# Optimization experiments

Hardware: AMD Instinct MI355X
Metric: run time of the kernel (lower is better)

## Reference

```python
import jax, jax.numpy as jnp
import numpy as np

DISTANCE_SCALE = 25.0
VIEW_PE = 6
STEP = 0.02  # nominal ray-march step size used to scale dists


def positional_encoding(positions, freqs):
    # matches torch: (positions[..., None] * 2**k).reshape(..., freqs*C) -> [sin, cos]
    freq_bands = 2.0 ** jnp.arange(freqs, dtype=positions.dtype)
    pts = (positions[..., None] * freq_bands).reshape(positions.shape[:-1] + (freqs * positions.shape[-1],))
    return jnp.concatenate([jnp.sin(pts), jnp.cos(pts)], axis=-1)


def setup_inputs() -> dict:
    key = jax.random.key(0)
    ks = jax.random.split(key, 10)
    n_rays, n_samples, C, featureC = 4096, 256, 27, 128
    in_mlpC = 3 + 2 * VIEW_PE * 3 + C  # 66
    density_features = jax.random.normal(ks[0], (n_rays, n_samples), jnp.float32)
    app_features = jax.random.normal(ks[1], (n_rays, n_samples, C), jnp.float32)
    viewdirs = jax.random.normal(ks[2], (n_rays, 3), jnp.float32)
    viewdirs = viewdirs / jnp.linalg.norm(viewdirs, axis=-1, keepdims=True)
    dists = jax.random.uniform(ks[3], (n_rays, n_samples), jnp.float32) * STEP
    s1 = 1.0 / np.sqrt(in_mlpC)
    s2 = 1.0 / np.sqrt(featureC)
    W1 = jax.random.uniform(ks[4], (in_mlpC, featureC), jnp.float32, -s1, s1)
    b1 = jax.random.uniform(ks[5], (featureC,), jnp.float32, -s1, s1)
    W2 = jax.random.uniform(ks[6], (featureC, featureC), jnp.float32, -s2, s2)
    b2 = jax.random.uniform(ks[7], (featureC,), jnp.float32, -s2, s2)
    W3 = jax.random.uniform(ks[8], (featureC, 3), jnp.float32, -s2, s2)
    b3 = jnp.zeros((3,), jnp.float32)  # torch init: constant_(bias, 0)
    return {"density_features": density_features, "app_features": app_features,
            "viewdirs": viewdirs, "dists": dists,
            "W1": W1, "b1": b1, "W2": W2, "b2": b2, "W3": W3, "b3": b3}


def reference(density_features, app_features, viewdirs, dists, W1, b1, W2, b2, W3, b3):
    # feature2density (relu activation)
    sigma = jax.nn.relu(density_features)  # [R, S]
    # raw2alpha
    alpha = 1.0 - jnp.exp(-sigma * dists * DISTANCE_SCALE)  # [R, S]
    T = jnp.cumprod(jnp.concatenate([jnp.ones((alpha.shape[0], 1), alpha.dtype),
                                     1.0 - alpha + 1e-10], axis=-1), axis=-1)
    weights = alpha * T[:, :-1]  # [R, S]
    # radiance MLP over all sample points
    R, S, C = app_features.shape
    vd = jnp.broadcast_to(viewdirs[:, None, :], (R, S, 3))
    mlp_in = jnp.concatenate([app_features, vd, positional_encoding(vd, VIEW_PE)], axis=-1)  # [R,S,66]
    h = jax.nn.relu(mlp_in @ W1 + b1)
    h = jax.nn.relu(h @ W2 + b2)
    rgb = jax.nn.sigmoid(h @ W3 + b3)  # [R, S, 3]
    # composite (white background)
    acc_map = jnp.sum(weights, axis=-1)  # [R]
    rgb_map = jnp.einsum('rs,rsc->rc', weights, rgb)  # [R, 3]
    rgb_map = jnp.clip(rgb_map + (1.0 - acc_map[:, None]), 0.0, 1.0)
    return rgb_map
```

## Files before the change

### kernel.cpp

```cpp
#include <hip/hip_runtime.h>
#include <hip/hip_bf16.h>

typedef float f32x4 __attribute__((ext_vector_type(4)));
typedef short s16x8 __attribute__((ext_vector_type(8)));
typedef unsigned int u32;
typedef u32 u32x2 __attribute__((ext_vector_type(2)));

#define DIST_SCALE 25.0f

__device__ __forceinline__ unsigned short f2b(float f) {
  union { float f; unsigned u; } v; v.f = f;
  unsigned r = v.u + 0x7fffu + ((v.u >> 16) & 1u);
  return (unsigned short)(r >> 16);
}

__device__ __forceinline__ u32 cvtpk(float lo, float hi) {
  u32 r;
  asm("v_cvt_pk_bf16_f32 %0, %1, %2" : "=v"(r) : "v"(lo), "v"(hi));
  return r;
}

__device__ __forceinline__ int swzH(int s, int chbyte) {
  return (s * 256 + chbyte) ^ ((s & 7) << 4);
}

__global__ void prep_weights(const float* __restrict__ W1, const float* __restrict__ W2,
                             const float* __restrict__ W3, unsigned short* __restrict__ ws) {
  int t = blockIdx.x * 256 + threadIdx.x;
  int stride = gridDim.x * 256;
  for (int i = t; i < 128 * 32; i += stride) {
    int n = i >> 5, k = i & 31;
    ws[i] = (k < 27) ? f2b(W1[k * 128 + n]) : (unsigned short)0;
  }
  unsigned short* w2t = ws + 4096;
  for (int i = t; i < 128 * 128; i += stride) {
    int n = i >> 7, k = i & 127;
    w2t[i] = f2b(W2[k * 128 + n]);
  }
  unsigned short* w3p = ws + 4096 + 16384;
  for (int i = t; i < 4 * 16 * 32; i += stride) {
    int wv = i >> 9, rem = i & 511, n = rem >> 5, ks = rem & 31;
    int kg = ks >> 3, j = ks & 7;
    int ch = wv * 32 + ((j >> 2) << 4) + kg * 4 + (j & 3);
    w3p[i] = (n < 3) ? f2b(W3[ch * 3 + n]) : (unsigned short)0;
  }
}

__global__ void __attribute__((amdgpu_waves_per_eu(4, 4))) __launch_bounds__(256) nerf_main(
    const float* __restrict__ dens, const float* __restrict__ app,
    const float* __restrict__ vdirs, const float* __restrict__ dists,
    const float* __restrict__ W1, const float* __restrict__ b1,
    const float* __restrict__ b2v, const float* __restrict__ b3v,
    const unsigned short* __restrict__ wsb, float* __restrict__ out) {
  __shared__ unsigned short Xs[64 * 40];
  __shared__ unsigned short HA[64 * 128];
  __shared__ float part[4 * 4 * 16 * 4];
  __shared__ float wbuf[256];
  __shared__ float hcbuf[128];
  __shared__ float featbuf[40];
  __shared__ float red[4][4];

  const int t = threadIdx.x;
  const int lane = t & 63;
  const int wv = t >> 6;
  const int r = blockIdx.x;

  const unsigned short* W1aT = wsb;
  const unsigned short* W2T = wsb + 4096;
  const unsigned short* W3P = wsb + 4096 + 16384;
  char* HAb = (char*)HA;

  const int cl = lane & 15;
  const int kg = lane >> 4;
  const int chBase = wv * 32;

  for (int i = t; i < 1280; i += 256) ((u32*)Xs)[i] = 0u;
  if (t < 39) {
    float val;
    if (t < 3) val = vdirs[r * 3 + t];
    else {
      int jj = t - 3;
      int trig = jj / 18;
      int rem = jj % 18;
      int c = rem / 6, k = rem % 6;
      float v = vdirs[r * 3 + c] * (float)(1 << k);
      val = trig ? cosf(v) : sinf(v);
    }
    featbuf[t] = val;
  }
  if (wv == 0) {
    const float4 dv = *(const float4*)(dens + (size_t)r * 256 + lane * 4);
    const float4 tv = *(const float4*)(dists + (size_t)r * 256 + lane * 4);
    float f[4], al[4];
    float dl[4] = {dv.x, dv.y, dv.z, dv.w};
    float tl[4] = {tv.x, tv.y, tv.z, tv.w};
    float p = 1.0f;
#pragma unroll
    for (int q = 0; q < 4; ++q) {
      float sg = fmaxf(dl[q], 0.0f);
      float e = __expf(-sg * tl[q] * DIST_SCALE);
      al[q] = 1.0f - e;
      f[q] = e + 1e-10f;
      p *= f[q];
    }
    float P = p;
#pragma unroll
    for (int dlt = 1; dlt < 64; dlt <<= 1) {
      float v = __shfl_up(P, dlt, 64);
      if (lane >= dlt) P *= v;
    }
    float E = __shfl_up(P, 1, 64);
    if (lane == 0) E = 1.0f;
    float tr = E;
#pragma unroll
    for (int q = 0; q < 4; ++q) { wbuf[lane * 4 + q] = al[q] * tr; tr *= f[q]; }
  }
  __syncthreads();
  if (t < 128) {
    float s = b1[t];
    for (int j = 0; j < 39; ++j) s += featbuf[j] * W1[(27 + j) * 128 + t];
    hcbuf[t] = s;
  }

  s16x8 w1f[2], w2f[2][4], w3s;
#pragma unroll
  for (int nt = 0; nt < 2; ++nt)
    w1f[nt] = *(const s16x8*)(W1aT + (chBase + nt * 16 + cl) * 32 + kg * 8);
#pragma unroll
  for (int nt = 0; nt < 2; ++nt)
#pragma unroll
    for (int kk = 0; kk < 4; ++kk)
      w2f[nt][kk] = *(const s16x8*)(W2T + (chBase + nt * 16 + cl) * 128 + kk * 32 + kg * 8);
  w3s = *(const s16x8*)(W3P + wv * 512 + cl * 32 + kg * 8);

  __syncthreads();

  float pr = 0.0f, pg = 0.0f, pb = 0.0f, pw = 0.0f;
  const float b30 = b3v[0], b31 = b3v[1], b32 = b3v[2];
  const f32x4 hc0 = *(const f32x4*)(hcbuf + chBase + kg * 4);
  const f32x4 hc1 = *(const f32x4*)(hcbuf + chBase + 16 + kg * 4);
  const f32x4 bb0 = *(const f32x4*)(b2v + chBase + kg * 4);
  const f32x4 bb1 = *(const f32x4*)(b2v + chBase + 16 + kg * 4);

  const float* rayBase = app + (size_t)r * 256 * 27;
  f32x4 L0 = *(const f32x4*)(rayBase + 4 * t);
  f32x4 L1 = {};
  if (t < 176) L1 = *(const f32x4*)(rayBase + 4 * (t + 256));

  for (int chunk = 0; chunk < 4; ++chunk) {
    const int sBase = chunk * 64;
    {
      int e0 = 4 * t;
#pragma unroll
      for (int u = 0; u < 4; ++u) {
        unsigned e = e0 + u;
        unsigned s = e / 27u, c = e - s * 27u;
        *(unsigned short*)((char*)Xs + s * 80 + 2 * c) = f2b(L0[u]);
      }
      if (t < 176) {
        int e1 = 4 * (t + 256);
#pragma unroll
        for (int u = 0; u < 4; ++u) {
          unsigned e = e1 + u;
          unsigned s = e / 27u, c = e - s * 27u;
          *(unsigned short*)((char*)Xs + s * 80 + 2 * c) = f2b(L1[u]);
        }
      }
    }
    __syncthreads();

    if (chunk < 3) {
      const float* slab = rayBase + (size_t)(chunk + 1) * 1728;
      L0 = *(const f32x4*)(slab + 4 * t);
      if (t < 176) L1 = *(const f32x4*)(slab + 4 * (t + 256));
    }

#pragma unroll
    for (int st = 0; st < 4; ++st) {
      const int s = st * 16 + cl;
      s16x8 xb = *(const s16x8*)((char*)Xs + s * 80 + kg * 16);
      f32x4 a0 = {}, a1 = {};
      a0 = __builtin_amdgcn_mfma_f32_16x16x32_bf16(w1f[0], xb, a0, 0, 0, 0);
      a1 = __builtin_amdgcn_mfma_f32_16x16x32_bf16(w1f[1], xb, a1, 0, 0, 0);
      u32x2 pk0 = {cvtpk(fmaxf(a0[0] + hc0[0], 0.0f), fmaxf(a0[1] + hc0[1], 0.0f)),
                   cvtpk(fmaxf(a0[2] + hc0[2], 0.0f), fmaxf(a0[3] + hc0[3], 0.0f))};
      u32x2 pk1 = {cvtpk(fmaxf(a1[0] + hc1[0], 0.0f), fmaxf(a1[1] + hc1[1], 0.0f)),
                   cvtpk(fmaxf(a1[2] + hc1[2], 0.0f), fmaxf(a1[3] + hc1[3], 0.0f))};
      *(u32x2*)(HAb + swzH(s, (chBase + kg * 4) * 2)) = pk0;
      *(u32x2*)(HAb + swzH(s, (chBase + 16 + kg * 4) * 2)) = pk1;
    }
    __syncthreads();

#pragma unroll
    for (int st = 0; st < 4; ++st) {
      const int s = st * 16 + cl;
      s16x8 hbf[4];
#pragma unroll
      for (int kk = 0; kk < 4; ++kk)
        hbf[kk] = *(const s16x8*)(HAb + swzH(s, (kk * 32 + kg * 8) * 2));
      f32x4 a0 = {}, a1 = {};
#pragma unroll
      for (int kk = 0; kk < 4; ++kk) {
        a0 = __builtin_amdgcn_mfma_f32_16x16x32_bf16(w2f[0][kk], hbf[kk], a0, 0, 0, 0);
        a1 = __builtin_amdgcn_mfma_f32_16x16x32_bf16(w2f[1][kk], hbf[kk], a1, 0, 0, 0);
      }
      union { u32 u[4]; s16x8 v; } b3;
      b3.u[0] = cvtpk(fmaxf(a0[0] + bb0[0], 0.0f), fmaxf(a0[1] + bb0[1], 0.0f));
      b3.u[1] = cvtpk(fmaxf(a0[2] + bb0[2], 0.0f), fmaxf(a0[3] + bb0[3], 0.0f));
      b3.u[2] = cvtpk(fmaxf(a1[0] + bb1[0], 0.0f), fmaxf(a1[1] + bb1[1], 0.0f));
      b3.u[3] = cvtpk(fmaxf(a1[2] + bb1[2], 0.0f), fmaxf(a1[3] + bb1[3], 0.0f));
      f32x4 p3 = {};
      p3 = __builtin_amdgcn_mfma_f32_16x16x32_bf16(w3s, b3.v, p3, 0, 0, 0);
      if (kg == 0)
        *(f32x4*)(part + ((wv * 4 + st) * 16 + cl) * 4) = p3;
    }
    __syncthreads();

    {
      f32x4 pv = *(const f32x4*)(part + ((kg * 4 + wv) * 16 + cl) * 4);
      float v0 = pv[0], v1 = pv[1], v2 = pv[2];
      v0 += __shfl_xor(v0, 16, 64); v0 += __shfl_xor(v0, 32, 64);
      v1 += __shfl_xor(v1, 16, 64); v1 += __shfl_xor(v1, 32, 64);
      v2 += __shfl_xor(v2, 16, 64); v2 += __shfl_xor(v2, 32, 64);
      if (kg == 0) {
        float w = wbuf[sBase + wv * 16 + cl];
        pw += w;
        pr += w / (1.0f + __expf(-(v0 + b30)));
        pg += w / (1.0f + __expf(-(v1 + b31)));
        pb += w / (1.0f + __expf(-(v2 + b32)));
      }
    }
  }

  if (kg == 0) {
#pragma unroll
    for (int d = 1; d < 16; d <<= 1) {
      pr += __shfl_xor(pr, d, 64);
      pg += __shfl_xor(pg, d, 64);
      pb += __shfl_xor(pb, d, 64);
      pw += __shfl_xor(pw, d, 64);
    }
    if (lane == 0) { red[wv][0] = pr; red[wv][1] = pg; red[wv][2] = pb; red[wv][3] = pw; }
  }
  __syncthreads();
  if (t == 0) {
    float R = 0, G = 0, B = 0, W = 0;
#pragma unroll
    for (int w = 0; w < 4; ++w) { R += red[w][0]; G += red[w][1]; B += red[w][2]; W += red[w][3]; }
    float bg = 1.0f - W;
    out[r * 3 + 0] = fminf(fmaxf(R + bg, 0.0f), 1.0f);
    out[r * 3 + 1] = fminf(fmaxf(G + bg, 0.0f), 1.0f);
    out[r * 3 + 2] = fminf(fmaxf(B + bg, 0.0f), 1.0f);
  }
}

extern "C" void kernel_launch(void* const* d_in, const int* in_sizes, int n_in,
                              void* d_out, int out_size, void* d_ws, size_t ws_size,
                              hipStream_t stream) {
  const float* dens = (const float*)d_in[0];
  const float* app  = (const float*)d_in[1];
  const float* vd   = (const float*)d_in[2];
  const float* dist = (const float*)d_in[3];
  const float* W1   = (const float*)d_in[4];
  const float* b1   = (const float*)d_in[5];
  const float* W2   = (const float*)d_in[6];
  const float* b2   = (const float*)d_in[7];
  const float* W3   = (const float*)d_in[8];
  const float* b3   = (const float*)d_in[9];
  unsigned short* wsb = (unsigned short*)d_ws;

  prep_weights<<<32, 256, 0, stream>>>(W1, W2, W3, wsb);
  nerf_main<<<4096, 256, 0, stream>>>(dens, app, vd, dist, W1, b1, b2, b3, wsb, (float*)d_out);
}
```

Baseline: 86.73 us.

## Split each ray block across eight waves with sixteen channels per wave

Doubles the block to 512 threads so each of eight waves owns 16 hidden channels instead of 32. W1/W2/W3 register fragments are halved, the W3 packing is redone for 16-channel slices, and the final partial sums from both wave halves are combined before the sigmoid. The aim is more parallelism per ray and lower register pressure per wave, with fewer serial MFMAs per wave. In exchange, the per-wave-pair partial buffer doubles, the third-layer MFMA runs half-empty, and more waves wait at each barrier.

```diff
diff --git a/kernel.cpp b/kernel.cpp
--- a/kernel.cpp
+++ b/kernel.cpp
@@ -38,15 +38,15 @@
     w2t[i] = f2b(W2[k * 128 + n]);
   }
   unsigned short* w3p = ws + 4096 + 16384;
-  for (int i = t; i < 4 * 16 * 32; i += stride) {
+  for (int i = t; i < 8 * 16 * 32; i += stride) {
     int wv = i >> 9, rem = i & 511, n = rem >> 5, ks = rem & 31;
     int kg = ks >> 3, j = ks & 7;
-    int ch = wv * 32 + ((j >> 2) << 4) + kg * 4 + (j & 3);
-    w3p[i] = (n < 3) ? f2b(W3[ch * 3 + n]) : (unsigned short)0;
-  }
-}
-
-__global__ void __attribute__((amdgpu_waves_per_eu(4, 4))) __launch_bounds__(256) nerf_main(
+    int ch = wv * 16 + kg * 4 + (j & 3);
+    w3p[i] = (n < 3 && j < 4) ? f2b(W3[ch * 3 + n]) : (unsigned short)0;
+  }
+}
+
+__global__ void __launch_bounds__(512, 6) nerf_main(
     const float* __restrict__ dens, const float* __restrict__ app,
     const float* __restrict__ vdirs, const float* __restrict__ dists,
     const float* __restrict__ W1, const float* __restrict__ b1,
@@ -54,7 +54,7 @@
     const unsigned short* __restrict__ wsb, float* __restrict__ out) {
   __shared__ unsigned short Xs[64 * 40];
   __shared__ unsigned short HA[64 * 128];
-  __shared__ float part[4 * 4 * 16 * 4];
+  __shared__ float part[8 * 4 * 16 * 4];
   __shared__ float wbuf[256];
   __shared__ float hcbuf[128];
   __shared__ float featbuf[40];
@@ -72,9 +72,11 @@
 
   const int cl = lane & 15;
   const int kg = lane >> 4;
-  const int chBase = wv * 32;
-
-  for (int i = t; i < 1280; i += 256) ((u32*)Xs)[i] = 0u;
+  const int ch16 = wv * 16;
+
+  const float* rayBase = app + (size_t)r * 6912;
+
+  for (int i = t; i < 1280; i += 512) ((u32*)Xs)[i] = 0u;
   if (t < 39) {
     float val;
     if (t < 3) val = vdirs[r * 3 + t];
@@ -122,34 +124,25 @@
     hcbuf[t] = s;
   }
 
-  s16x8 w1f[2], w2f[2][4], w3s;
-#pragma unroll
-  for (int nt = 0; nt < 2; ++nt)
-    w1f[nt] = *(const s16x8*)(W1aT + (chBase + nt * 16 + cl) * 32 + kg * 8);
-#pragma unroll
-  for (int nt = 0; nt < 2; ++nt)
-#pragma unroll
-    for (int kk = 0; kk < 4; ++kk)
-      w2f[nt][kk] = *(const s16x8*)(W2T + (chBase + nt * 16 + cl) * 128 + kk * 32 + kg * 8);
+  s16x8 w1f, w2f[4], w3s;
+  w1f = *(const s16x8*)(W1aT + (ch16 + cl) * 32 + kg * 8);
+#pragma unroll
+  for (int kk = 0; kk < 4; ++kk)
+    w2f[kk] = *(const s16x8*)(W2T + (ch16 + cl) * 128 + kk * 32 + kg * 8);
   w3s = *(const s16x8*)(W3P + wv * 512 + cl * 32 + kg * 8);
 
+  const f32x4 bb0 = *(const f32x4*)(b2v + ch16 + kg * 4);
+  const float b30 = b3v[0], b31 = b3v[1], b32 = b3v[2];
+  float pr = 0.0f, pg = 0.0f, pb = 0.0f, pw = 0.0f;
+
   __syncthreads();
-
-  float pr = 0.0f, pg = 0.0f, pb = 0.0f, pw = 0.0f;
-  const float b30 = b3v[0], b31 = b3v[1], b32 = b3v[2];
-  const f32x4 hc0 = *(const f32x4*)(hcbuf + chBase + kg * 4);
-  const f32x4 hc1 = *(const f32x4*)(hcbuf + chBase + 16 + kg * 4);
-  const f32x4 bb0 = *(const f32x4*)(b2v + chBase + kg * 4);
-  const f32x4 bb1 = *(const f32x4*)(b2v + chBase + 16 + kg * 4);
-
-  const float* rayBase = app + (size_t)r * 256 * 27;
-  f32x4 L0 = *(const f32x4*)(rayBase + 4 * t);
-  f32x4 L1 = {};
-  if (t < 176) L1 = *(const f32x4*)(rayBase + 4 * (t + 256));
+  const f32x4 hc0 = *(const f32x4*)(hcbuf + ch16 + kg * 4);
+
+  f32x4 L0 = {};
+  if (t < 432) L0 = *(const f32x4*)(rayBase + 4 * t);
 
   for (int chunk = 0; chunk < 4; ++chunk) {
-    const int sBase = chunk * 64;
-    {
+    if (t < 432) {
       int e0 = 4 * t;
 #pragma unroll
       for (int u = 0; u < 4; ++u) {
@@ -157,58 +150,43 @@
         unsigned s = e / 27u, c = e - s * 27u;
         *(unsigned short*)((char*)Xs + s * 80 + 2 * c) = f2b(L0[u]);
       }
-      if (t < 176) {
-        int e1 = 4 * (t + 256);
-#pragma unroll
-        for (int u = 0; u < 4; ++u) {
-          unsigned e = e1 + u;
-          unsigned s = e / 27u, c = e - s * 27u;
-          *(unsigned short*)((char*)Xs + s * 80 + 2 * c) = f2b(L1[u]);
-        }
-      }
     }
     __syncthreads();
 
-    if (chunk < 3) {
-      const float* slab = rayBase + (size_t)(chunk + 1) * 1728;
-      L0 = *(const f32x4*)(slab + 4 * t);
-      if (t < 176) L1 = *(const f32x4*)(slab + 4 * (t + 256));
-    }
+    if (chunk < 3 && t < 432)
+      L0 = *(const f32x4*)(rayBase + (size_t)(chunk + 1) * 1728 + 4 * t);
 
 #pragma unroll
     for (int st = 0; st < 4; ++st) {
       const int s = st * 16 + cl;
       s16x8 xb = *(const s16x8*)((char*)Xs + s * 80 + kg * 16);
-      f32x4 a0 = {}, a1 = {};
-      a0 = __builtin_amdgcn_mfma_f32_16x16x32_bf16(w1f[0], xb, a0, 0, 0, 0);
-      a1 = __builtin_amdgcn_mfma_f32_16x16x32_bf16(w1f[1], xb, a1, 0, 0, 0);
+      f32x4 a0 = {};
+      a0 = __builtin_amdgcn_mfma_f32_16x16x32_bf16(w1f, xb, a0, 0, 0, 0);
       u32x2 pk0 = {cvtpk(fmaxf(a0[0] + hc0[0], 0.0f), fmaxf(a0[1] + hc0[1], 0.0f)),
                    cvtpk(fmaxf(a0[2] + hc0[2], 0.0f), fmaxf(a0[3] + hc0[3], 0.0f))};
-      u32x2 pk1 = {cvtpk(fmaxf(a1[0] + hc1[0], 0.0f), fmaxf(a1[1] + hc1[1], 0.0f)),
-                   cvtpk(fmaxf(a1[2] + hc1[2], 0.0f), fmaxf(a1[3] + hc1[3], 0.0f))};
-      *(u32x2*)(HAb + swzH(s, (chBase + kg * 4) * 2)) = pk0;
-      *(u32x2*)(HAb + swzH(s, (chBase + 16 + kg * 4) * 2)) = pk1;
+      *(u32x2*)(HAb + swzH(s, (ch16 + kg * 4) * 2)) = pk0;
     }
     __syncthreads();
 
 #pragma unroll
     for (int st = 0; st < 4; ++st) {
       const int s = st * 16 + cl;
-      s16x8 hbf[4];
-#pragma unroll
-      for (int kk = 0; kk < 4; ++kk)
-        hbf[kk] = *(const s16x8*)(HAb + swzH(s, (kk * 32 + kg * 8) * 2));
-      f32x4 a0 = {}, a1 = {};
-#pragma unroll
-      for (int kk = 0; kk < 4; ++kk) {
-        a0 = __builtin_amdgcn_mfma_f32_16x16x32_bf16(w2f[0][kk], hbf[kk], a0, 0, 0, 0);
-        a1 = __builtin_amdgcn_mfma_f32_16x16x32_bf16(w2f[1][kk], hbf[kk], a1, 0, 0, 0);
+      f32x4 a0 = {};
+      {
+        s16x8 h0 = *(const s16x8*)(HAb + swzH(s, (0 * 32 + kg * 8) * 2));
+        s16x8 h1 = *(const s16x8*)(HAb + swzH(s, (1 * 32 + kg * 8) * 2));
+        a0 = __builtin_amdgcn_mfma_f32_16x16x32_bf16(w2f[0], h0, a0, 0, 0, 0);
+        a0 = __builtin_amdgcn_mfma_f32_16x16x32_bf16(w2f[1], h1, a0, 0, 0, 0);
+        h0 = *(const s16x8*)(HAb + swzH(s, (2 * 32 + kg * 8) * 2));
+        h1 = *(const s16x8*)(HAb + swzH(s, (3 * 32 + kg * 8) * 2));
+        a0 = __builtin_amdgcn_mfma_f32_16x16x32_bf16(w2f[2], h0, a0, 0, 0, 0);
+        a0 = __builtin_amdgcn_mfma_f32_16x16x32_bf16(w2f[3], h1, a0, 0, 0, 0);
       }
       union { u32 u[4]; s16x8 v; } b3;
       b3.u[0] = cvtpk(fmaxf(a0[0] + bb0[0], 0.0f), fmaxf(a0[1] + bb0[1], 0.0f));
       b3.u[1] = cvtpk(fmaxf(a0[2] + bb0[2], 0.0f), fmaxf(a0[3] + bb0[3], 0.0f));
-      b3.u[2] = cvtpk(fmaxf(a1[0] + bb1[0], 0.0f), fmaxf(a1[1] + bb1[1], 0.0f));
-      b3.u[3] = cvtpk(fmaxf(a1[2] + bb1[2], 0.0f), fmaxf(a1[3] + bb1[3], 0.0f));
+      b3.u[2] = 0u;
+      b3.u[3] = 0u;
       f32x4 p3 = {};
       p3 = __builtin_amdgcn_mfma_f32_16x16x32_bf16(w3s, b3.v, p3, 0, 0, 0);
       if (kg == 0)
@@ -216,14 +194,17 @@
     }
     __syncthreads();
 
-    {
-      f32x4 pv = *(const f32x4*)(part + ((kg * 4 + wv) * 16 + cl) * 4);
-      float v0 = pv[0], v1 = pv[1], v2 = pv[2];
+    if (wv < 4) {
+      f32x4 pa = *(const f32x4*)(part + ((kg * 4 + wv) * 16 + cl) * 4);
+      f32x4 pb4 = *(const f32x4*)(part + (((kg + 4) * 4 + wv) * 16 + cl) * 4);
+      float v0 = pa[0] + pb4[0];
+      float v1 = pa[1] + pb4[1];
+      float v2 = pa[2] + pb4[2];
       v0 += __shfl_xor(v0, 16, 64); v0 += __shfl_xor(v0, 32, 64);
       v1 += __shfl_xor(v1, 16, 64); v1 += __shfl_xor(v1, 32, 64);
       v2 += __shfl_xor(v2, 16, 64); v2 += __shfl_xor(v2, 32, 64);
       if (kg == 0) {
-        float w = wbuf[sBase + wv * 16 + cl];
+        float w = wbuf[chunk * 64 + wv * 16 + cl];
         pw += w;
         pr += w / (1.0f + __expf(-(v0 + b30)));
         pg += w / (1.0f + __expf(-(v1 + b31)));
@@ -232,7 +213,7 @@
     }
   }
 
-  if (kg == 0) {
+  if (wv < 4 && kg == 0) {
 #pragma unroll
     for (int d = 1; d < 16; d <<= 1) {
       pr += __shfl_xor(pr, d, 64);
@@ -270,5 +251,5 @@
   unsigned short* wsb = (unsigned short*)d_ws;
 
   prep_weights<<<32, 256, 0, stream>>>(W1, W2, W3, wsb);
-  nerf_main<<<4096, 256, 0, stream>>>(dens, app, vd, dist, W1, b1, b2, b3, wsb, (float*)d_out);
-}
+  nerf_main<<<4096, 512, 0, stream>>>(dens, app, vd, dist, W1, b1, b2, b3, wsb, (float*)d_out);
+}
```

Result: slower. 110.4 us (+27.3%).
